# Optimization experiments

Measured on AMD Instinct MI355X. Metric: run time of the kernel, lower is better.

Reference implementation:

```python
import jax, jax.numpy as jnp
import numpy as np

DT_SCALER = 1.0 / 24
COVAR_INDEX = np.array([0] + list(range(7, 25)))
INSULIN_INDEX = np.array(list(range(1, 6)))
T = 100          # SEQUENCE_LENGTH
B = 512
H = 256          # hidden_dim
ODE_H = 50       # hidden width of the ODE MLP (hardcoded in cODERNN_)
ODE_STEPS = 8    # fixed-step RK4 stands in for adaptive dopri5 (rtol=atol=1e-3)


def setup_inputs() -> dict:
    key = jax.random.key(0)
    ks = jax.random.split(key, 24)
    std = 0.1
    d = {}
    d["dt"] = jax.random.uniform(ks[0], (B, T, 2), jnp.float32)
    d["x"] = jax.random.normal(ks[1], (B, T, 25), jnp.float32)
    # rnn1: RNNCell(19, H)
    d["Wih1"] = std * jax.random.normal(ks[2], (H, 19), jnp.float32)
    d["Whh1"] = std * jax.random.normal(ks[3], (H, H), jnp.float32)
    d["bih1"] = jnp.zeros((H,), jnp.float32)
    d["bhh1"] = jnp.zeros((H,), jnp.float32)
    # rnn2: RNNCell(5+H, H)
    d["Wih2"] = std * jax.random.normal(ks[4], (H, 5 + H), jnp.float32)
    d["Whh2"] = std * jax.random.normal(ks[5], (H, H), jnp.float32)
    d["bih2"] = jnp.zeros((H,), jnp.float32)
    d["bhh2"] = jnp.zeros((H,), jnp.float32)
    # output_net_covar: Linear(H,H) -> tanh -> Linear(H,1)
    d["oW1"] = std * jax.random.normal(ks[6], (H, H), jnp.float32)
    d["ob1"] = jnp.zeros((H,), jnp.float32)
    d["oW2"] = std * jax.random.normal(ks[7], (1, H), jnp.float32)
    d["ob2"] = jnp.zeros((1,), jnp.float32)
    # output_net_insulin: Linear(H,H) -> tanh -> Linear(H,1) -> relu
    d["iW1"] = std * jax.random.normal(ks[8], (H, H), jnp.float32)
    d["ib1"] = jnp.zeros((H,), jnp.float32)
    d["iW2"] = std * jax.random.normal(ks[9], (1, H), jnp.float32)
    d["ib2"] = jnp.zeros((1,), jnp.float32)
    # ODE func net: Linear(H,50) -> tanh -> Linear(50,H)
    d["fW1"] = std * jax.random.normal(ks[10], (ODE_H, H), jnp.float32)
    d["fb1"] = jnp.zeros((ODE_H,), jnp.float32)
    d["fW2"] = std * jax.random.normal(ks[11], (H, ODE_H), jnp.float32)
    d["fb2"] = jnp.zeros((H,), jnp.float32)
    return d


def _rnn_cell(x, h, Wih, Whh, bih, bhh):
    return jnp.tanh(x @ Wih.T + bih + h @ Whh.T + bhh)


def _solve_ode(h0, scale, fW1, fb1, fW2, fb2):
    """Integrate dh/ds = net(h) * scale over s in [0,1] with fixed-step RK4.
    scale = dt_i * DT_SCALER, shape [B,1]."""
    hs = 1.0 / ODE_STEPS

    def f(h):
        return (jnp.tanh(h @ fW1.T + fb1) @ fW2.T + fb2) * scale

    def step(h, _):
        k1 = f(h)
        k2 = f(h + 0.5 * hs * k1)
        k3 = f(h + 0.5 * hs * k2)
        k4 = f(h + hs * k3)
        return h + (hs / 6.0) * (k1 + 2 * k2 + 2 * k3 + k4), None

    h, _ = jax.lax.scan(step, h0, None, length=ODE_STEPS)
    return h


def reference(dt, x, Wih1, Whh1, bih1, bhh1, Wih2, Whh2, bih2, bhh2,
              oW1, ob1, oW2, ob2, iW1, ib1, iW2, ib2, fW1, fb1, fW2, fb2):
    Bb, Tt, _ = x.shape
    x_ins = x[:, :, INSULIN_INDEX]      # [B,T,5]
    x_cov = x[:, :, COVAR_INDEX]        # [B,T,19]
    treat = (jnp.sum(x_ins > 0, axis=2, keepdims=True) > 0).astype(x.dtype)  # [B,T,1]
    dt_i = (dt[:, :, 1] - dt[:, :, 0])[..., None]                            # [B,T,1]

    def out_cov(h):
        return jnp.tanh(h @ oW1.T + ob1) @ oW2.T + ob2

    def out_ins(h):
        return jax.nn.relu(jnp.tanh(h @ iW1.T + ib1) @ iW2.T + ib2)

    def step(carry, inp):
        h_cov, h_ins = carry
        xc, xi, d, tr = inp             # [B,19],[B,5],[B,1],[B,1]
        h_cov = h_cov + _rnn_cell(xc, h_cov, Wih1, Whh1, bih1, bhh1)
        h_ins = h_ins + _rnn_cell(jnp.concatenate([xi, h_cov], axis=1), h_ins,
                                  Wih2, Whh2, bih2, bhh2)
        scale = d * DT_SCALER
        h_cov = _solve_ode(h_cov, scale, fW1, fb1, fW2, fb2)
        h_ins = _solve_ode(h_ins, scale, fW1, fb1, fW2, fb2)
        mu = out_cov(h_cov) - tr * out_ins(h_ins)   # [B,1]
        return (h_cov, h_ins), mu

    Hd = Whh1.shape[0]
    init = (jnp.zeros((Bb, Hd), x.dtype), jnp.zeros((Bb, Hd), x.dtype))
    xs = (jnp.swapaxes(x_cov, 0, 1), jnp.swapaxes(x_ins, 0, 1),
          jnp.swapaxes(dt_i, 0, 1), jnp.swapaxes(treat, 0, 1))
    _, mus = jax.lax.scan(step, init, xs)           # [T,B,1]
    return jnp.swapaxes(mus[:, :, 0], 0, 1)        # [B,T]
```

## Files before the change

### kernel.cpp

```cpp
#include <hip/hip_runtime.h>

#define TT 100
#define NSTEP 8
__device__ __constant__ float kDT_SC = 1.0f / 24.0f;
#define HS (0.125f)

typedef float f4 __attribute__((ext_vector_type(4)));
typedef float f2 __attribute__((ext_vector_type(2)));

#define OFF_WHH1T4   0
#define OFF_WIH1T    65536
#define OFF_WIH2AT   70656
#define OFF_WIH2BT4  72704
#define OFF_WHH2T4   138240
#define OFF_OW1T4    203776
#define OFF_IW1T4    269312
#define OFF_FW1R     334848
#define OFF_FW2T4    351232
#define OFF_B1C      364544
#define OFF_B2C      364800
#define WS_FLOATS    365056

#define L_YC    0
#define L_Z     2176
#define L_PART  2432
#define L_XA    3456
#define L_TR    3512
#define L_RED   3514
#define L_TOTAL 3530

__device__ __forceinline__ float fast_tanh(float v) {
    float e = __expf(2.0f * v);
    return 1.0f - 2.0f / (e + 1.0f);
}
__device__ __forceinline__ f2 vlo(f4 v) { return __builtin_shufflevector(v, v, 0, 1); }
__device__ __forceinline__ f2 vhi(f4 v) { return __builtin_shufflevector(v, v, 2, 3); }
__device__ __forceinline__ void pkfma(f2& a, f2 w, f2 h) {
    a = __builtin_elementwise_fma(w, h, a);
}
__device__ __forceinline__ float rsum2(f2 a) { return a.x + a.y; }
__device__ __forceinline__ int yi4(int jb) { return (jb >> 4) * 17 + (jb & 15); }

template <int CTRL>
__device__ __forceinline__ float dpp_rr_add(float v) {
    int r = __builtin_amdgcn_update_dpp(0, __float_as_int(v), CTRL, 0xF, 0xF, false);
    return v + __int_as_float(r);
}
__device__ __forceinline__ float allreduce16(float v) {
    v = dpp_rr_add<0x121>(v);
    v = dpp_rr_add<0x122>(v);
    v = dpp_rr_add<0x124>(v);
    v = dpp_rr_add<0x128>(v);
    return v;
}

__global__ void codernn_setup(const float* __restrict__ Wih1, const float* __restrict__ Whh1,
                              const float* __restrict__ bih1, const float* __restrict__ bhh1,
                              const float* __restrict__ Wih2, const float* __restrict__ Whh2,
                              const float* __restrict__ bih2, const float* __restrict__ bhh2,
                              const float* __restrict__ oW1, const float* __restrict__ iW1,
                              const float* __restrict__ fW1, const float* __restrict__ fW2,
                              float* __restrict__ ws) {
    int e = blockIdx.x * 256 + threadIdx.x;
    if (e >= WS_FLOATS) return;
    float v;
    if (e < OFF_WIH1T) {
        int q = e; int jb = q >> 10, i = (q >> 2) & 255, dj = q & 3;
        v = Whh1[i * 256 + jb * 4 + dj];
    } else if (e < OFF_WIH2AT) {
        int q = e - OFF_WIH1T; int j = q >> 8, i = q & 255;
        v = (j < 19) ? Wih1[i * 19 + j] : 0.0f;
    } else if (e < OFF_WIH2BT4) {
        int q = e - OFF_WIH2AT; int j = q >> 8, i = q & 255;
        v = (j < 5) ? Wih2[i * 261 + j] : 0.0f;
    } else if (e < OFF_WHH2T4) {
        int q = e - OFF_WIH2BT4; int jb = q >> 10, i = (q >> 2) & 255, dj = q & 3;
        v = Wih2[i * 261 + 5 + jb * 4 + dj];
    } else if (e < OFF_OW1T4) {
        int q = e - OFF_WHH2T4; int jb = q >> 10, i = (q >> 2) & 255, dj = q & 3;
        v = Whh2[i * 256 + jb * 4 + dj];
    } else if (e < OFF_IW1T4) {
        int q = e - OFF_OW1T4; int jb = q >> 10, i = (q >> 2) & 255, dj = q & 3;
        v = oW1[i * 256 + jb * 4 + dj];
    } else if (e < OFF_FW1R) {
        int q = e - OFF_IW1T4; int jb = q >> 10, i = (q >> 2) & 255, dj = q & 3;
        v = iW1[i * 256 + jb * 4 + dj];
    } else if (e < OFF_FW2T4) {
        int q = e - OFF_FW1R; int k = q >> 8, j = q & 255;
        v = (k < 50) ? fW1[k * 256 + j] : 0.0f;
    } else if (e < OFF_B1C) {
        int q = e - OFF_FW2T4; int kb = q >> 10, i = (q >> 2) & 255, dk = q & 3;
        int k = kb * 4 + dk;
        v = (k < 50) ? fW2[i * 50 + k] : 0.0f;
    } else if (e < OFF_B2C) {
        int q = e - OFF_B1C; v = bih1[q] + bhh1[q];
    } else {
        int q = e - OFF_B2C; v = bih2[q] + bhh2[q];
    }
    ws[e] = v;
}

#define ZPHASE(EL) { \
    float pz[8]; \
    _Pragma("unroll") for (int s = 0; s < 2; ++s) { \
        const f4* ys = ycur4 + (EL) * 136 + s * 68 + (p16 >> 2) * 17 + (p16 & 3) * 4; \
        f2 P0l={0,0},P0h={0,0},P1l={0,0},P1h={0,0},P2l={0,0},P2h={0,0},P3l={0,0},P3h={0,0}; \
        _Pragma("unroll") for (int m = 0; m < 4; ++m) { \
            f4 y = ys[m]; f2 yl = vlo(y), yh = vhi(y); \
            pkfma(P0l, vlo(cache[m]), yl);      pkfma(P0h, vhi(cache[m]), yh); \
            pkfma(P1l, vlo(cache[4+m]), yl);    pkfma(P1h, vhi(cache[4+m]), yh); \
            pkfma(P2l, vlo(cache[8+m]), yl);    pkfma(P2h, vhi(cache[8+m]), yh); \
            pkfma(P3l, vlo(cache[12+m]), yl);   pkfma(P3h, vhi(cache[12+m]), yh); } \
        pz[s*4+0]=rsum2(P0l+P0h); pz[s*4+1]=rsum2(P1l+P1h); \
        pz[s*4+2]=rsum2(P2l+P2h); pz[s*4+3]=rsum2(P3l+P3h); } \
    _Pragma("unroll") for (int r = 0; r < 8; ++r) pz[r] = allreduce16(pz[r]); \
    if (p16 < 8) { const int q = p16; \
        float a0=(q&1)?pz[1]:pz[0]; float a1=(q&1)?pz[3]:pz[2]; \
        float a2=(q&1)?pz[5]:pz[4]; float a3=(q&1)?pz[7]:pz[6]; \
        float b0s=(q&2)?a1:a0; float b1s=(q&2)?a3:a2; float vsum=(q&4)?b1s:b0s; \
        float fz0=(q&1)?fb1r[1]:fb1r[0]; float fz1=(q&1)?fb1r[3]:fb1r[2]; float fb=(q&2)?fz1:fz0; \
        sm[L_Z + (EL)*128 + (q>>2)*64 + 4*kg + (q&3)] = fast_tanh(vsum + fb); } \
}

#define UPDATE(EL, SG, Y00, Y01, AC0, AC1, SCV) { \
    const f4* zva = (const f4*)(sm + L_Z + (EL) * 128); \
    const f4* zvb = zva + 16; \
    f2 AL={0,0},AH={0,0},BL={0,0},BH={0,0}; \
    _Pragma("unroll") for (int kb = 0; kb < 13; ++kb) { \
        f4 w = cache[kb]; f4 za = zva[kb], zb = zvb[kb]; \
        pkfma(AL, vlo(w), vlo(za)); pkfma(AH, vhi(w), vhi(za)); \
        pkfma(BL, vlo(w), vlo(zb)); pkfma(BH, vhi(w), vhi(zb)); } \
    float du0 = (fb2i + rsum2(AL + AH)) * (SCV); \
    float du1 = (fb2i + rsum2(BL + BH)) * (SCV); \
    float yn0, yn1; \
    if ((SG) == 0)      { AC0 = du0; AC1 = du1; yn0 = fmaf(0.5f*HS, du0, Y00); yn1 = fmaf(0.5f*HS, du1, Y01); } \
    else if ((SG) == 1) { AC0 = fmaf(2.f, du0, AC0); AC1 = fmaf(2.f, du1, AC1); yn0 = fmaf(0.5f*HS, du0, Y00); yn1 = fmaf(0.5f*HS, du1, Y01); } \
    else if ((SG) == 2) { AC0 = fmaf(2.f, du0, AC0); AC1 = fmaf(2.f, du1, AC1); yn0 = fmaf(HS, du0, Y00); yn1 = fmaf(HS, du1, Y01); } \
    else { AC0 += du0; AC1 += du1; Y00 = fmaf(HS/6.f, AC0, Y00); Y01 = fmaf(HS/6.f, AC1, Y01); yn0 = Y00; yn1 = Y01; } \
    sm[L_YC + (EL)*544 + yslot] = yn0; \
    sm[L_YC + (EL)*544 + 272 + yslot] = yn1; \
}

__global__ __launch_bounds__(512, 2) void codernn_main(
    const float* __restrict__ dt, const float* __restrict__ x,
    const float* __restrict__ ws,
    const float* __restrict__ ob1, const float* __restrict__ oW2, const float* __restrict__ ob2,
    const float* __restrict__ ib1, const float* __restrict__ iW2, const float* __restrict__ ib2,
    const float* __restrict__ fb1, const float* __restrict__ fb2,
    float* __restrict__ out) {
    __shared__ float sm[L_TOTAL];
    const int tid = threadIdx.x;
    const int i = tid & 255;
    const int sh = tid >> 8;
    const int bgA = blockIdx.x * 2, bgB = bgA + 1;
    const int lane = tid & 63, wv = tid >> 6;
    const int kg = (tid >> 4) & 15;
    const int p16 = tid & 15;

    for (int idx = tid; idx < 1088; idx += 512) sm[L_YC + idx] = 0.0f;

    const float b1ci = ws[OFF_B1C + i];
    const float b2ci = ws[OFF_B2C + i];
    const float fb2i = fb2[i];
    const float W2sel = sh ? iW2[i] : oW2[i];
    const float b1sel = sh ? ib1[i] : ob1[i];
    const float ob2s = ob2[0], ib2s = ib2[0];

    const f4* Whh1T4  = (const f4*)(ws + OFF_WHH1T4);
    const float* Wih1T  = ws + OFF_WIH1T;
    const float* Wih2aT = ws + OFF_WIH2AT;
    const f4* Wih2bT4 = (const f4*)(ws + OFF_WIH2BT4);
    const f4* Whh2T4  = (const f4*)(ws + OFF_WHH2T4);
    const f4* oW1T4   = (const f4*)(ws + OFF_OW1T4);
    const f4* iW1T4   = (const f4*)(ws + OFF_IW1T4);
    const f4* ycur4   = (const f4*)(sm + L_YC);

    f4 cache[16];
    if (sh == 0) {
        const f4* g = (const f4*)(ws + OFF_FW1R);
        #pragma unroll
        for (int r = 0; r < 4; ++r)
            #pragma unroll
            for (int m = 0; m < 4; ++m)
                cache[r * 4 + m] = g[(4 * kg + r) * 64 + p16 * 4 + m];
    } else {
        const f4* g = (const f4*)(ws + OFF_FW2T4);
        #pragma unroll
        for (int kb = 0; kb < 13; ++kb) cache[kb] = g[kb * 256 + i];
        cache[13] = (f4){0,0,0,0}; cache[14] = (f4){0,0,0,0}; cache[15] = (f4){0,0,0,0};
    }
    float fb1r[4];
    #pragma unroll
    for (int r = 0; r < 4; ++r) fb1r[r] = (4 * kg + r < 50) ? fb1[4 * kg + r] : 0.0f;

    const int yslot = (i >> 6) * 68 + (i & 63);

    float y0A0 = 0.f, y0A1 = 0.f, y0B0 = 0.f, y0B1 = 0.f;
    float accA0, accA1, accB0, accB1;
    __syncthreads();

    for (int t = 0; t < TT; ++t) {
        if (tid < 56) {
            int bb = tid / 28, c = tid - bb * 28;
            const float* xp = x + (bgA + bb) * (TT * 25) + t * 25;
            sm[L_XA + tid] = (c < 25) ? xp[c] : 0.0f;
            if (c == 25)
                sm[L_TR + bb] = (xp[1] > 0.f || xp[2] > 0.f || xp[3] > 0.f || xp[4] > 0.f || xp[5] > 0.f) ? 1.0f : 0.0f;
        }
        const float scA = (dt[bgA * (TT * 2) + t * 2 + 1] - dt[bgA * (TT * 2) + t * 2]) * kDT_SC;
        const float scB = (dt[bgB * (TT * 2) + t * 2 + 1] - dt[bgB * (TT * 2) + t * 2]) * kDT_SC;
        __syncthreads();

        {
            float xpA = 0.f, xpB = 0.f;
            if (sh == 0) {
                xpA = fmaf(Wih1T[i], sm[L_XA + 0], b1ci);
                xpB = fmaf(Wih1T[i], sm[L_XA + 28 + 0], b1ci);
                #pragma unroll
                for (int j = 1; j < 19; ++j) {
                    float w = Wih1T[j * 256 + i];
                    xpA = fmaf(w, sm[L_XA + 6 + j], xpA);
                    xpB = fmaf(w, sm[L_XA + 28 + 6 + j], xpB);
                }
            }
            const int jb0 = sh * 32;
            f2 aLA={0,0},aHA={0,0},aLB={0,0},aHB={0,0};
            #pragma unroll 4
            for (int jb = 0; jb < 32; ++jb) {
                f4 w = Whh1T4[(jb0 + jb) * 256 + i];
                f4 hA = ycur4[yi4(jb0 + jb)];
                f4 hB = ycur4[136 + yi4(jb0 + jb)];
                pkfma(aLA, vlo(w), vlo(hA)); pkfma(aHA, vhi(w), vhi(hA));
                pkfma(aLB, vlo(w), vlo(hB)); pkfma(aHB, vhi(w), vhi(hB));
            }
            sm[L_PART + sh * 256 + i] = xpA + rsum2(aLA + aHA);
            sm[L_PART + 512 + sh * 256 + i] = xpB + rsum2(aLB + aHB);
        }
        __syncthreads();
        if (sh == 1) {
            y0A0 = y0A0 + fast_tanh(sm[L_PART + i] + sm[L_PART + 256 + i]);
            sm[L_YC + yslot] = y0A0;
            y0B0 = y0B0 + fast_tanh(sm[L_PART + 512 + i] + sm[L_PART + 768 + i]);
            sm[L_YC + 544 + yslot] = y0B0;
        }
        __syncthreads();

        {
            float xpA = 0.f, xpB = 0.f;
            if (sh == 0) {
                xpA = b2ci; xpB = b2ci;
                #pragma unroll
                for (int j = 0; j < 5; ++j) {
                    float w = Wih2aT[j * 256 + i];
                    xpA = fmaf(w, sm[L_XA + 1 + j], xpA);
                    xpB = fmaf(w, sm[L_XA + 28 + 1 + j], xpB);
                }
            }
            const f4* Wp = sh ? Whh2T4 : Wih2bT4;
            const int stsel = sh;
            f2 aLA={0,0},aHA={0,0},aLB={0,0},aHB={0,0};
            #pragma unroll 4
            for (int jb = 0; jb < 64; ++jb) {
                f4 w = Wp[jb * 256 + i];
                f4 hA = ycur4[stsel * 68 + yi4(jb)];
                f4 hB = ycur4[136 + stsel * 68 + yi4(jb)];
                pkfma(aLA, vlo(w), vlo(hA)); pkfma(aHA, vhi(w), vhi(hA));
                pkfma(aLB, vlo(w), vlo(hB)); pkfma(aHB, vhi(w), vhi(hB));
            }
            sm[L_PART + sh * 256 + i] = xpA + rsum2(aLA + aHA);
            sm[L_PART + 512 + sh * 256 + i] = xpB + rsum2(aLB + aHB);
        }
        __syncthreads();
        if (sh == 1) {
            y0A1 = y0A1 + fast_tanh(sm[L_PART + i] + sm[L_PART + 256 + i]);
            sm[L_YC + 272 + yslot] = y0A1;
            y0B1 = y0B1 + fast_tanh(sm[L_PART + 512 + i] + sm[L_PART + 768 + i]);
            sm[L_YC + 544 + 272 + yslot] = y0B1;
        }
        __syncthreads();

        if (sh == 0) ZPHASE(0);
        __syncthreads();
        for (int st = 0; st < NSTEP; ++st) {
            #pragma unroll
            for (int sg = 0; sg < 4; ++sg) {
                if (sh == 0) { ZPHASE(1); }
                else         { UPDATE(0, sg, y0A0, y0A1, accA0, accA1, scA); }
                __syncthreads();
                if (sh == 0) { ZPHASE(0); }
                else         { UPDATE(1, sg, y0B0, y0B1, accB0, accB1, scB); }
                __syncthreads();
            }
        }

        {
            const f4* Wh = sh ? iW1T4 : oW1T4;
            const int stsel = sh;
            f2 aLA={0,0},aHA={0,0},aLB={0,0},aHB={0,0};
            #pragma unroll 4
            for (int jb = 0; jb < 64; ++jb) {
                f4 w = Wh[jb * 256 + i];
                f4 hA = ycur4[stsel * 68 + yi4(jb)];
                f4 hB = ycur4[136 + stsel * 68 + yi4(jb)];
                pkfma(aLA, vlo(w), vlo(hA)); pkfma(aHA, vhi(w), vhi(hA));
                pkfma(aLB, vlo(w), vlo(hB)); pkfma(aHB, vhi(w), vhi(hB));
            }
            float vA = W2sel * fast_tanh(b1sel + rsum2(aLA + aHA));
            float vB = W2sel * fast_tanh(b1sel + rsum2(aLB + aHB));
            #pragma unroll
            for (int off = 32; off > 0; off >>= 1) {
                vA += __shfl_xor(vA, off);
                vB += __shfl_xor(vB, off);
            }
            if (lane == 0) { sm[L_RED + wv * 2] = vA; sm[L_RED + wv * 2 + 1] = vB; }
        }
        __syncthreads();
        if (tid == 0) {
            float coA = sm[L_RED + 0] + sm[L_RED + 2] + sm[L_RED + 4] + sm[L_RED + 6] + ob2s;
            float ciA = sm[L_RED + 8] + sm[L_RED + 10] + sm[L_RED + 12] + sm[L_RED + 14] + ib2s;
            out[bgA * TT + t] = coA - sm[L_TR] * fmaxf(ciA, 0.0f);
            float coB = sm[L_RED + 1] + sm[L_RED + 3] + sm[L_RED + 5] + sm[L_RED + 7] + ob2s;
            float ciB = sm[L_RED + 9] + sm[L_RED + 11] + sm[L_RED + 13] + sm[L_RED + 15] + ib2s;
            out[bgB * TT + t] = coB - sm[L_TR + 1] * fmaxf(ciB, 0.0f);
        }
        __syncthreads();
    }
}

extern "C" void kernel_launch(void* const* d_in, const int* in_sizes, int n_in,
                              void* d_out, int out_size, void* d_ws, size_t ws_size,
                              hipStream_t stream) {
    const float* dt   = (const float*)d_in[0];
    const float* x    = (const float*)d_in[1];
    const float* Wih1 = (const float*)d_in[2];
    const float* Whh1 = (const float*)d_in[3];
    const float* bih1 = (const float*)d_in[4];
    const float* bhh1 = (const float*)d_in[5];
    const float* Wih2 = (const float*)d_in[6];
    const float* Whh2 = (const float*)d_in[7];
    const float* bih2 = (const float*)d_in[8];
    const float* bhh2 = (const float*)d_in[9];
    const float* oW1  = (const float*)d_in[10];
    const float* ob1  = (const float*)d_in[11];
    const float* oW2  = (const float*)d_in[12];
    const float* ob2  = (const float*)d_in[13];
    const float* iW1  = (const float*)d_in[14];
    const float* ib1  = (const float*)d_in[15];
    const float* iW2  = (const float*)d_in[16];
    const float* ib2  = (const float*)d_in[17];
    const float* fW1  = (const float*)d_in[18];
    const float* fb1  = (const float*)d_in[19];
    const float* fW2  = (const float*)d_in[20];
    const float* fb2  = (const float*)d_in[21];
    float* ws  = (float*)d_ws;
    float* out = (float*)d_out;

    if (ws_size < (size_t)WS_FLOATS * sizeof(float)) return;

    codernn_setup<<<WS_FLOATS / 256, 256, 0, stream>>>(Wih1, Whh1, bih1, bhh1, Wih2, Whh2,
                                                       bih2, bhh2, oW1, iW1, fW1, fW2, ws);

    codernn_main<<<256, 512, 0, stream>>>(dt, x, ws,
                                          ob1, oW2, ob2, ib1, iW2, ib2, fb1, fb2, out);
}
```

Baseline: 5.273 ms.

## Replace ODE-loop block barriers with LDS flag producer/consumer handshakes

Inside the RK4 stage loop, the two half-blocks previously met at a full __syncthreads after every Z-phase and state update. They now signal each other through four counters in LDS. Each wave's lane 0 bumps a counter with a workgroup-scope release atomic, and the consumer spins with acquire loads plus s_sleep. The goal is to cut full-block barrier cost and let each half wait only on the data it actually needs. The price is spin-wait overhead, and correctness now rests on getting the flag targets and LDS memory ordering right.

```diff
diff --git a/kernel.cpp b/kernel.cpp
--- a/kernel.cpp
+++ b/kernel.cpp
@@ -27,7 +27,8 @@
 #define L_XA    3456
 #define L_TR    3512
 #define L_RED   3514
-#define L_TOTAL 3530
+#define L_FLAG  3530
+#define L_TOTAL 3534
 
 __device__ __forceinline__ float fast_tanh(float v) {
     float e = __expf(2.0f * v);
@@ -52,6 +53,15 @@
     v = dpp_rr_add<0x124>(v);
     v = dpp_rr_add<0x128>(v);
     return v;
+}
+
+__device__ __forceinline__ void waitFlag(unsigned int* f, unsigned int target) {
+    while (__hip_atomic_load(f, __ATOMIC_ACQUIRE, __HIP_MEMORY_SCOPE_WORKGROUP) < target)
+        __builtin_amdgcn_s_sleep(1);
+}
+__device__ __forceinline__ void incFlag(unsigned int* f, int lane) {
+    if (lane == 0)
+        __hip_atomic_fetch_add(f, 1u, __ATOMIC_RELEASE, __HIP_MEMORY_SCOPE_WORKGROUP);
 }
 
 __global__ void codernn_setup(const float* __restrict__ Wih1, const float* __restrict__ Whh1,
@@ -149,6 +159,7 @@
     const float* __restrict__ fb1, const float* __restrict__ fb2,
     float* __restrict__ out) {
     __shared__ float sm[L_TOTAL];
+    unsigned int* flg = (unsigned int*)&sm[L_FLAG];
     const int tid = threadIdx.x;
     const int i = tid & 255;
     const int sh = tid >> 8;
@@ -207,6 +218,7 @@
             if (c == 25)
                 sm[L_TR + bb] = (xp[1] > 0.f || xp[2] > 0.f || xp[3] > 0.f || xp[4] > 0.f || xp[5] > 0.f) ? 1.0f : 0.0f;
         }
+        if (tid >= 60 && tid < 64) flg[tid - 60] = 0u;
         const float scA = (dt[bgA * (TT * 2) + t * 2 + 1] - dt[bgA * (TT * 2) + t * 2]) * kDT_SC;
         const float scB = (dt[bgB * (TT * 2) + t * 2 + 1] - dt[bgB * (TT * 2) + t * 2]) * kDT_SC;
         __syncthreads();
@@ -279,19 +291,34 @@
         }
         __syncthreads();
 
-        if (sh == 0) ZPHASE(0);
-        __syncthreads();
-        for (int st = 0; st < NSTEP; ++st) {
-            #pragma unroll
-            for (int sg = 0; sg < 4; ++sg) {
-                if (sh == 0) { ZPHASE(1); }
-                else         { UPDATE(0, sg, y0A0, y0A1, accA0, accA1, scA); }
-                __syncthreads();
-                if (sh == 0) { ZPHASE(0); }
-                else         { UPDATE(1, sg, y0B0, y0B1, accB0, accB1, scB); }
-                __syncthreads();
-            }
-        }
+        if (sh == 0) {
+            for (int st = 0; st < NSTEP; ++st) {
+                #pragma unroll
+                for (int sg = 0; sg < 4; ++sg) {
+                    const unsigned int e = (unsigned int)(st * 4 + sg);
+                    waitFlag(flg + 2, 4u * e);
+                    ZPHASE(0);
+                    incFlag(flg + 0, lane);
+                    waitFlag(flg + 3, 4u * e);
+                    ZPHASE(1);
+                    incFlag(flg + 1, lane);
+                }
+            }
+        } else {
+            for (int st = 0; st < NSTEP; ++st) {
+                #pragma unroll
+                for (int sg = 0; sg < 4; ++sg) {
+                    const unsigned int e = (unsigned int)(st * 4 + sg);
+                    waitFlag(flg + 0, 4u * (e + 1));
+                    UPDATE(0, sg, y0A0, y0A1, accA0, accA1, scA);
+                    incFlag(flg + 2, lane);
+                    waitFlag(flg + 1, 4u * (e + 1));
+                    UPDATE(1, sg, y0B0, y0B1, accB0, accB1, scB);
+                    incFlag(flg + 3, lane);
+                }
+            }
+        }
+        __syncthreads();
 
         {
             const f4* Wh = sh ? iW1T4 : oW1T4;
```

After: 5.296 ms. About the same (+0.4%).
